# Optimization experiments

Hardware: AMD Instinct MI355X
Metric: run time of the kernel (lower is better)

## Reference

```python
import jax, jax.numpy as jnp
import numpy as np

B_, N, C, NH, NW = 2048, 64, 512, 16, 64  # N == window_size

def setup_inputs() -> dict:
    key = jax.random.key(0)
    k0, k1, k2, k3 = jax.random.split(key, 4)
    std = 0.02
    return {
        "inputs": jax.random.normal(k0, (B_, N, C), jnp.float32),
        "mask": jnp.zeros((NW, N, N), jnp.float32),  # (0 / -inf) additive window mask
        "qkv_w": jax.random.normal(k1, (3 * C, C), jnp.float32) * std,
        "qkv_b": jnp.zeros((3 * C,), jnp.float32),
        "proj_w": jax.random.normal(k2, (C, C), jnp.float32) * std,
        "proj_b": jnp.zeros((C,), jnp.float32),
        "bias_table": jax.random.normal(k3, (2 * N - 1, NH), jnp.float32) * std,
    }

def reference(inputs, mask, qkv_w, qkv_b, proj_w, proj_b, bias_table):
    b, n, c = inputs.shape
    nh = bias_table.shape[1]
    hd = c // nh
    scale = hd ** -0.5
    # qkv projection -> (3, B_, nh, N, hd)
    qkv = (inputs @ qkv_w.T + qkv_b).reshape(b, n, 3, nh, hd).transpose(2, 0, 3, 1, 4)
    q, k, v = qkv[0] * scale, qkv[1], qkv[2]
    attn = jnp.einsum('bhqd,bhkd->bhqk', q, k)  # (B_, nh, N, N)
    # 1D relative position bias, gathered from table
    rel_idx = jnp.arange(n)[:, None] - jnp.arange(n)[None, :] + (n - 1)  # (N, N)
    rel_bias = bias_table[rel_idx]                 # (N, N, nh)
    attn = attn + rel_bias.transpose(2, 0, 1)[None]  # add (nh, N, N)
    # additive window mask
    nw = mask.shape[0]
    attn = attn.reshape(b // nw, nw, nh, n, n) + mask[None, :, None]
    attn = jax.nn.softmax(attn.reshape(b, nh, n, n), axis=-1)
    out = jnp.einsum('bhqk,bhkd->bqhd', attn, v).reshape(b, n, c)
    return out @ proj_w.T + proj_b
```

## Files before the change

### kernel.cpp

```cpp
#include <hip/hip_runtime.h>

typedef __bf16 bf16x8 __attribute__((ext_vector_type(8)));
typedef float f32x4 __attribute__((ext_vector_type(4)));

__device__ __forceinline__ unsigned short f2bf(float x) {
  union { float f; unsigned int u; } c; c.f = x;
  unsigned int r = c.u + 0x7FFFu + ((c.u >> 16) & 1u);
  return (unsigned short)(r >> 16);
}

__global__ __launch_bounds__(256) void f32_to_bf16_vec4(
    const float* __restrict__ in, unsigned short* __restrict__ out, int n4) {
  int i = blockIdx.x * blockDim.x + threadIdx.x;
  int stride = gridDim.x * blockDim.x;
  const float4* in4 = (const float4*)in;
  ushort4* out4 = (ushort4*)out;
  for (; i < n4; i += stride) {
    float4 f = in4[i];
    ushort4 u;
    u.x = f2bf(f.x); u.y = f2bf(f.y); u.z = f2bf(f.z); u.w = f2bf(f.w);
    out4[i] = u;
  }
}

__global__ __launch_bounds__(256) void build_bias_mask_frag(
    const float* __restrict__ bias_table,
    const float* __restrict__ mask,
    float* __restrict__ Mc) {
  const int idx = blockIdx.x * 256 + threadIdx.x;
  const int j = idx & 15, lane = (idx >> 4) & 63, mt = (idx >> 10) & 3;
  const int h = (idx >> 12) & 15, w = idx >> 16;
  const int r = j >> 2, nt = j & 3, lg = lane >> 4, lr = lane & 15;
  const int q = mt * 16 + lg * 4 + r, k = nt * 16 + lr;
  Mc[idx] = bias_table[(q - k + 63) * 16 + h] + mask[(w * 64 + q) * 64 + k];
}

#define GLOAD_LDS16(gp, lp)                                                          \
  __builtin_amdgcn_global_load_lds(                                                  \
      (const __attribute__((address_space(1))) unsigned int*)(uintptr_t)(gp),        \
      (__attribute__((address_space(3))) unsigned int*)(uintptr_t)(lp), 16, 0, 0)

template <int NBN, int EPI>
__global__ __launch_bounds__(512, 2) void gemm256(
    const unsigned short* __restrict__ A,
    const unsigned short* __restrict__ B,
    const float* __restrict__ bias,
    void* __restrict__ C0, void* __restrict__ C1, void* __restrict__ C2,
    int ldc) {
  constexpr int K = 512;
  constexpr int NT = K / 64;
  __shared__ __attribute__((aligned(128))) char lds[131072];

  const int t = threadIdx.x;
  const int lane = t & 63;
  const int wid = t >> 6;
  const int wr = wid >> 2, wc = wid & 3;
  const int lr = lane & 15, lg = lane >> 4;

  const int nwg = gridDim.x;
  const int cpx = nwg >> 3;
  const int wgid = (blockIdx.x & 7) * cpx + (blockIdx.x >> 3);
  const int bm = wgid / NBN, bn = wgid % NBN;
  const int m0 = bm * 256, n0 = bn * 256;

  const char* Ab = (const char*)(A + (size_t)m0 * K);
  const char* Bb = (const char*)(B + (size_t)n0 * K);

  const int r3 = t >> 3, ps = t & 7;

  unsigned aoff[2][2], adst[2][2], boff[2][2], bdst[2][2];
#pragma unroll
  for (int j = 0; j < 2; ++j)
#pragma unroll
    for (int i = 0; i < 2; ++i) {
      const int rowA = i * 128 + j * 64 + r3;
      aoff[j][i] = (unsigned)((rowA * K + ((ps ^ (rowA & 7)) << 3)) * 2);
      adst[j][i] = (unsigned)(rowA * 128 + ps * 16);
      const int rowB = i * 128 + ((r3 >> 5) << 6) + j * 32 + (r3 & 31);
      boff[j][i] = (unsigned)((rowB * K + ((ps ^ (rowB & 7)) << 3)) * 2);
      bdst[j][i] = (unsigned)(65536 + rowB * 128 + ps * 16);
    }

#define STAGE_A(j, tt, buf)                                                   \
  do {                                                                        \
    GLOAD_LDS16(Ab + aoff[j][0] + (tt)*128, lds + (buf)*32768 + adst[j][0]);  \
    GLOAD_LDS16(Ab + aoff[j][1] + (tt)*128, lds + (buf)*32768 + adst[j][1]);  \
  } while (0)
#define STAGE_B(j, tt, buf)                                                   \
  do {                                                                        \
    GLOAD_LDS16(Bb + boff[j][0] + (tt)*128, lds + (buf)*32768 + bdst[j][0]);  \
    GLOAD_LDS16(Bb + boff[j][1] + (tt)*128, lds + (buf)*32768 + bdst[j][1]);  \
  } while (0)

  unsigned abase[2], bbase[2];
#pragma unroll
  for (int kk = 0; kk < 2; ++kk) {
    abase[kk] = (unsigned)((wr * 128 + lr) * 128 + (((kk * 4 + lg) ^ (lr & 7)) << 4));
    bbase[kk] = (unsigned)(65536 + (wc * 64 + lr) * 128 + (((kk * 4 + lg) ^ (lr & 7)) << 4));
  }

  f32x4 acc[8][4];
#pragma unroll
  for (int i = 0; i < 8; ++i)
#pragma unroll
    for (int j = 0; j < 4; ++j) acc[i][j] = f32x4{0.f, 0.f, 0.f, 0.f};

#define BAR_IN()                                         \
  __builtin_amdgcn_s_barrier();                          \
  asm volatile("s_waitcnt lgkmcnt(0)" ::: "memory");     \
  __builtin_amdgcn_sched_barrier(0);                     \
  __builtin_amdgcn_s_setprio(1)
#define MFMA16(QM, NTLO)                                                            \
  _Pragma("unroll") for (int mt = 0; mt < 4; ++mt)                                  \
    _Pragma("unroll") for (int nt = 0; nt < 2; ++nt)                                \
      _Pragma("unroll") for (int kk = 0; kk < 2; ++kk)                              \
        acc[(QM)*4 + mt][(NTLO) + nt] = __builtin_amdgcn_mfma_f32_16x16x32_bf16(    \
            af[mt][kk], bfr[(NTLO) + nt][kk], acc[(QM)*4 + mt][(NTLO) + nt], 0, 0, 0)

  STAGE_A(0, 0, 0); STAGE_B(0, 0, 0); STAGE_B(1, 0, 0); STAGE_A(1, 0, 0);
  STAGE_A(0, 1, 1); STAGE_B(0, 1, 1); STAGE_B(1, 1, 1); STAGE_A(1, 1, 1);
  asm volatile("s_waitcnt vmcnt(8)" ::: "memory");
  __builtin_amdgcn_s_barrier();

#pragma unroll
  for (int tt = 0; tt < NT; ++tt) {
    const int buf = tt & 1;
    bf16x8 af[4][2], bfr[4][2];
#pragma unroll
    for (int nt = 0; nt < 2; ++nt)
#pragma unroll
      for (int kk = 0; kk < 2; ++kk)
        bfr[nt][kk] = *(const bf16x8*)(lds + buf * 32768 + bbase[kk] + nt * 2048);
#pragma unroll
    for (int mt = 0; mt < 4; ++mt)
#pragma unroll
      for (int kk = 0; kk < 2; ++kk)
        af[mt][kk] = *(const bf16x8*)(lds + buf * 32768 + abase[kk] + mt * 2048);
    BAR_IN();
    MFMA16(0, 0);
    __builtin_amdgcn_s_setprio(0);
    __builtin_amdgcn_s_barrier();
#pragma unroll
    for (int nt = 2; nt < 4; ++nt)
#pragma unroll
      for (int kk = 0; kk < 2; ++kk)
        bfr[nt][kk] = *(const bf16x8*)(lds + buf * 32768 + bbase[kk] + nt * 2048);
    if (tt + 2 < NT) { STAGE_A(0, tt + 2, buf); STAGE_B(0, tt + 2, buf); }
    BAR_IN();
    MFMA16(0, 2);
    __builtin_amdgcn_s_setprio(0);
    __builtin_amdgcn_s_barrier();
#pragma unroll
    for (int mt = 0; mt < 4; ++mt)
#pragma unroll
      for (int kk = 0; kk < 2; ++kk)
        af[mt][kk] = *(const bf16x8*)(lds + buf * 32768 + abase[kk] + 8192 + mt * 2048);
    if (tt + 2 < NT) STAGE_B(1, tt + 2, buf);
    BAR_IN();
    MFMA16(1, 0);
    __builtin_amdgcn_s_setprio(0);
    __builtin_amdgcn_s_barrier();
    if (tt + 2 < NT) STAGE_A(1, tt + 2, buf);
    BAR_IN();
    MFMA16(1, 2);
    __builtin_amdgcn_s_setprio(0);
    if (tt + 2 < NT)      asm volatile("s_waitcnt vmcnt(8)" ::: "memory");
    else if (tt == NT - 2) asm volatile("s_waitcnt vmcnt(0)" ::: "memory");
    __builtin_amdgcn_s_barrier();
  }
#undef MFMA16
#undef BAR_IN
#undef STAGE_A
#undef STAGE_B

#pragma unroll
  for (int qm = 0; qm < 2; ++qm)
#pragma unroll
    for (int mt = 0; mt < 4; ++mt)
#pragma unroll
      for (int nt = 0; nt < 4; ++nt) {
        const int n = n0 + wc * 64 + nt * 16 + lr;
        const float bv = bias[n];
        const f32x4 a4 = acc[qm * 4 + mt][nt];
        if constexpr (EPI == 2) {
          const int part = n >> 9;
          unsigned short* dst = part == 0 ? (unsigned short*)C0
                                 : (part == 1 ? (unsigned short*)C1 : (unsigned short*)C2);
          const float sc = (part == 0) ? 0.17677669529663687f : 1.0f;
          const int hh = (n >> 5) & 15, dd = n & 31;
#pragma unroll
          for (int r = 0; r < 4; ++r) {
            const int m = m0 + wr * 128 + qm * 64 + mt * 16 + lg * 4 + r;
            dst[((size_t)((m >> 6) * 16 + hh) * 64 + (m & 63)) * 32 + dd] =
                f2bf((a4[r] + bv) * sc);
          }
        } else {
#pragma unroll
          for (int r = 0; r < 4; ++r) {
            const int m = m0 + wr * 128 + qm * 64 + mt * 16 + lg * 4 + r;
            ((float*)C0)[(size_t)m * ldc + n] = a4[r] + bv;
          }
        }
      }
}

__global__ __launch_bounds__(128) void attn_kernel(
    const unsigned short* __restrict__ Qh,
    const unsigned short* __restrict__ Kh,
    const unsigned short* __restrict__ Vh,
    const float* __restrict__ Mc,
    unsigned short* __restrict__ attn_out
) {
  const int wv = threadIdx.x >> 6;
  const int bh = blockIdx.x * 2 + wv;
  const int b = bh >> 4, h = bh & 15;
  const int lane = threadIdx.x & 63;
  const int lr = lane & 15, lg = lane >> 4;

  __shared__ unsigned short VtS[2][32 * 72];
  __shared__ unsigned short PlS[2][16 * 72];
  unsigned short* Vt = VtS[wv];
  unsigned short* Pl = PlS[wv];

  const unsigned short* qb = Qh + (size_t)bh * 2048;
  const unsigned short* kb = Kh + (size_t)bh * 2048;
  const unsigned short* vg = Vh + (size_t)bh * 2048;

  bf16x8 vr[4];
#pragma unroll
  for (int i = 0; i < 4; ++i) vr[i] = ((const bf16x8*)(vg + lane * 32))[i];
  bf16x8 kf[4], qf[4];
#pragma unroll
  for (int nt = 0; nt < 4; ++nt)
    kf[nt] = *(const bf16x8*)(kb + (nt * 16 + lr) * 32 + lg * 8);
#pragma unroll
  for (int mt = 0; mt < 4; ++mt)
    qf[mt] = *(const bf16x8*)(qb + (mt * 16 + lr) * 32 + lg * 8);

  {
    __bf16* vt = (__bf16*)Vt;
#pragma unroll
    for (int d = 0; d < 8; ++d) {
      vt[(d)*72 + lane] = vr[0][d];
      vt[(d + 8) * 72 + lane] = vr[1][d];
      vt[(d + 16) * 72 + lane] = vr[2][d];
      vt[(d + 24) * 72 + lane] = vr[3][d];
    }
  }
  bf16x8 vfrag[2][2];
#pragma unroll
  for (int dt = 0; dt < 2; ++dt)
#pragma unroll
    for (int ki = 0; ki < 2; ++ki)
      vfrag[dt][ki] = *(const bf16x8*)(Vt + (dt * 16 + lr) * 72 + ki * 32 + lg * 8);

  const float* Mb = Mc + ((size_t)((b & 63) * 16 + h) * 4) * 1024 + lane * 16;

  f32x4 o[4][2];
#pragma unroll
  for (int i = 0; i < 4; ++i)
#pragma unroll
    for (int j = 0; j < 2; ++j) o[i][j] = f32x4{0.f, 0.f, 0.f, 0.f};
  float rinv[4][4];

#pragma unroll
  for (int mt = 0; mt < 4; ++mt) {
    f32x4 mv4[4];
#pragma unroll
    for (int j = 0; j < 4; ++j)
      mv4[j] = ((const f32x4*)(Mb + (size_t)mt * 1024))[j];

    f32x4 s[4];
#pragma unroll
    for (int nt = 0; nt < 4; ++nt) s[nt] = f32x4{0.f, 0.f, 0.f, 0.f};
#pragma unroll
    for (int nt = 0; nt < 4; ++nt)
      s[nt] = __builtin_amdgcn_mfma_f32_16x16x32_bf16(qf[mt], kf[nt], s[nt], 0, 0, 0);

#pragma unroll
    for (int r = 0; r < 4; ++r) {
      float v[4];
      float sum = 0.f;
#pragma unroll
      for (int nt = 0; nt < 4; ++nt) {
        v[nt] = __expf(s[nt][r] + mv4[r][nt]);
        sum += v[nt];
      }
      sum += __shfl_xor(sum, 1, 64);
      sum += __shfl_xor(sum, 2, 64);
      sum += __shfl_xor(sum, 4, 64);
      sum += __shfl_xor(sum, 8, 64);
      rinv[mt][r] = __builtin_amdgcn_rcpf(sum);
#pragma unroll
      for (int nt = 0; nt < 4; ++nt)
        Pl[(lg * 4 + r) * 72 + nt * 16 + lr] = f2bf(v[nt]);
    }

    bf16x8 pa[2];
#pragma unroll
    for (int ki = 0; ki < 2; ++ki)
      pa[ki] = *(const bf16x8*)(Pl + lr * 72 + ki * 32 + lg * 8);
#pragma unroll
    for (int dt = 0; dt < 2; ++dt)
#pragma unroll
      for (int ki = 0; ki < 2; ++ki)
        o[mt][dt] = __builtin_amdgcn_mfma_f32_16x16x32_bf16(pa[ki], vfrag[dt][ki], o[mt][dt], 0, 0, 0);
  }

#pragma unroll
  for (int mt = 0; mt < 4; ++mt) {
#pragma unroll
    for (int r = 0; r < 4; ++r) {
      const int m = mt * 16 + lg * 4 + r;
      const float ri = rinv[mt][r];
#pragma unroll
      for (int dt = 0; dt < 2; ++dt) {
        const int d = dt * 16 + lr;
        attn_out[(size_t)(b * 64 + m) * 512 + h * 32 + d] = f2bf(o[mt][dt][r] * ri);
      }
    }
  }
}

extern "C" void kernel_launch(void* const* d_in, const int* in_sizes, int n_in,
                              void* d_out, int out_size, void* d_ws, size_t ws_size,
                              hipStream_t stream) {
  const float* X = (const float*)d_in[0];
  const float* mask = (const float*)d_in[1];
  const float* qkv_w = (const float*)d_in[2];
  const float* qkv_b = (const float*)d_in[3];
  const float* proj_w = (const float*)d_in[4];
  const float* proj_b = (const float*)d_in[5];
  const float* bias_table = (const float*)d_in[6];
  float* out = (float*)d_out;
  char* ws = (char*)d_ws;

  unsigned short* Xb      = (unsigned short*)(ws);
  unsigned short* Qh      = (unsigned short*)(ws + 134217728ull);
  unsigned short* Kh      = (unsigned short*)(ws + 268435456ull);
  unsigned short* Vh      = (unsigned short*)(ws + 402653184ull);
  unsigned short* attnout = (unsigned short*)(ws + 536870912ull);
  unsigned short* qkv_wb  = (unsigned short*)(ws + 671088640ull);
  unsigned short* proj_wb = (unsigned short*)(ws + 672661504ull);
  float*          Mf      = (float*)(ws + 673185792ull);

  f32_to_bf16_vec4<<<2048, 256, 0, stream>>>(X, Xb, 67108864 / 4);
  f32_to_bf16_vec4<<<768, 256, 0, stream>>>(qkv_w, qkv_wb, 786432 / 4);
  f32_to_bf16_vec4<<<256, 256, 0, stream>>>(proj_w, proj_wb, 262144 / 4);
  build_bias_mask_frag<<<16384, 256, 0, stream>>>(bias_table, mask, Mf);

  gemm256<6, 2><<<3072, 512, 0, stream>>>(Xb, qkv_wb, qkv_b, (void*)Qh, (void*)Kh, (void*)Vh, 1536);

  attn_kernel<<<16384, 128, 0, stream>>>(Qh, Kh, Vh, Mf, attnout);

  gemm256<2, 0><<<1024, 512, 0, stream>>>(attnout, proj_wb, proj_b, (void*)out, nullptr, nullptr, 512);
}
```

Baseline: 635.6 us.

## Rebalance GEMM prefetch schedule and transpose attention scores for cheaper softmax

The GEMM main loop now prefetches the second half of the next K tile into the other buffer during the current iteration and the first half two iterations ahead, with adjusted vmcnt waits. This spreads global-to-LDS loads more evenly across the MFMA phases. The attention kernel computes S transposed (K×Q), so each lane holds four key values for one query row. That cuts the row-sum reduction to two cross-lane shuffles, lets P be normalised before packing with v_cvt_pk_bf16_f32 and written as 8-byte stores, and removes the final rescale. The bias/mask fragment layout is permuted to match, and the new wait counts carry a risk of ordering errors.

```diff
diff --git a/kernel.cpp b/kernel.cpp
--- a/kernel.cpp
+++ b/kernel.cpp
@@ -7,6 +7,12 @@
   union { float f; unsigned int u; } c; c.f = x;
   unsigned int r = c.u + 0x7FFFu + ((c.u >> 16) & 1u);
   return (unsigned short)(r >> 16);
+}
+
+__device__ __forceinline__ unsigned int cvt_pk_bf16(float a, float b) {
+  unsigned int r;
+  asm("v_cvt_pk_bf16_f32 %0, %1, %2" : "=v"(r) : "v"(a), "v"(b));
+  return r;
 }
 
 __global__ __launch_bounds__(256) void f32_to_bf16_vec4(
@@ -30,8 +36,8 @@
   const int idx = blockIdx.x * 256 + threadIdx.x;
   const int j = idx & 15, lane = (idx >> 4) & 63, mt = (idx >> 10) & 3;
   const int h = (idx >> 12) & 15, w = idx >> 16;
-  const int r = j >> 2, nt = j & 3, lg = lane >> 4, lr = lane & 15;
-  const int q = mt * 16 + lg * 4 + r, k = nt * 16 + lr;
+  const int nt = j >> 2, r = j & 3, lg = lane >> 4, lr = lane & 15;
+  const int q = mt * 16 + lr, k = nt * 16 + lg * 4 + r;
   Mc[idx] = bias_table[(q - k + 63) * 16 + h] + mask[(w * 64 + q) * 64 + k];
 }
 
@@ -118,13 +124,14 @@
             af[mt][kk], bfr[(NTLO) + nt][kk], acc[(QM)*4 + mt][(NTLO) + nt], 0, 0, 0)
 
   STAGE_A(0, 0, 0); STAGE_B(0, 0, 0); STAGE_B(1, 0, 0); STAGE_A(1, 0, 0);
-  STAGE_A(0, 1, 1); STAGE_B(0, 1, 1); STAGE_B(1, 1, 1); STAGE_A(1, 1, 1);
+  STAGE_A(0, 1, 1); STAGE_B(0, 1, 1);
   asm volatile("s_waitcnt vmcnt(8)" ::: "memory");
   __builtin_amdgcn_s_barrier();
 
 #pragma unroll
   for (int tt = 0; tt < NT; ++tt) {
     const int buf = tt & 1;
+    const int nb = buf ^ 1;
     bf16x8 af[4][2], bfr[4][2];
 #pragma unroll
     for (int nt = 0; nt < 2; ++nt)
@@ -136,36 +143,42 @@
 #pragma unroll
       for (int kk = 0; kk < 2; ++kk)
         af[mt][kk] = *(const bf16x8*)(lds + buf * 32768 + abase[kk] + mt * 2048);
+    if (tt + 1 < NT) STAGE_B(1, tt + 1, nb);
     BAR_IN();
     MFMA16(0, 0);
     __builtin_amdgcn_s_setprio(0);
+    if (tt == NT - 1) asm volatile("s_waitcnt vmcnt(2)" ::: "memory");
+    else              asm volatile("s_waitcnt vmcnt(8)" ::: "memory");
     __builtin_amdgcn_s_barrier();
 #pragma unroll
     for (int nt = 2; nt < 4; ++nt)
 #pragma unroll
       for (int kk = 0; kk < 2; ++kk)
         bfr[nt][kk] = *(const bf16x8*)(lds + buf * 32768 + bbase[kk] + nt * 2048);
-    if (tt + 2 < NT) { STAGE_A(0, tt + 2, buf); STAGE_B(0, tt + 2, buf); }
+    if (tt + 1 < NT) STAGE_A(1, tt + 1, nb);
     BAR_IN();
     MFMA16(0, 2);
     __builtin_amdgcn_s_setprio(0);
+    if (tt == NT - 1) asm volatile("s_waitcnt vmcnt(0)" ::: "memory");
+    else              asm volatile("s_waitcnt vmcnt(8)" ::: "memory");
     __builtin_amdgcn_s_barrier();
 #pragma unroll
     for (int mt = 0; mt < 4; ++mt)
 #pragma unroll
       for (int kk = 0; kk < 2; ++kk)
         af[mt][kk] = *(const bf16x8*)(lds + buf * 32768 + abase[kk] + 8192 + mt * 2048);
-    if (tt + 2 < NT) STAGE_B(1, tt + 2, buf);
+    if (tt + 2 < NT) STAGE_A(0, tt + 2, buf);
     BAR_IN();
     MFMA16(1, 0);
     __builtin_amdgcn_s_setprio(0);
+    if (tt < NT - 1) asm volatile("s_waitcnt vmcnt(8)" ::: "memory");
     __builtin_amdgcn_s_barrier();
-    if (tt + 2 < NT) STAGE_A(1, tt + 2, buf);
+    if (tt + 2 < NT) STAGE_B(0, tt + 2, buf);
     BAR_IN();
     MFMA16(1, 2);
     __builtin_amdgcn_s_setprio(0);
-    if (tt + 2 < NT)      asm volatile("s_waitcnt vmcnt(8)" ::: "memory");
-    else if (tt == NT - 2) asm volatile("s_waitcnt vmcnt(0)" ::: "memory");
+    if (tt < NT - 2)       asm volatile("s_waitcnt vmcnt(8)" ::: "memory");
+    else if (tt == NT - 2) asm volatile("s_waitcnt vmcnt(4)" ::: "memory");
     __builtin_amdgcn_s_barrier();
   }
 #undef MFMA16
@@ -261,39 +274,42 @@
   for (int i = 0; i < 4; ++i)
 #pragma unroll
     for (int j = 0; j < 2; ++j) o[i][j] = f32x4{0.f, 0.f, 0.f, 0.f};
-  float rinv[4][4];
 
 #pragma unroll
   for (int mt = 0; mt < 4; ++mt) {
-    f32x4 mv4[4];
-#pragma unroll
-    for (int j = 0; j < 4; ++j)
-      mv4[j] = ((const f32x4*)(Mb + (size_t)mt * 1024))[j];
-
-    f32x4 s[4];
-#pragma unroll
-    for (int nt = 0; nt < 4; ++nt) s[nt] = f32x4{0.f, 0.f, 0.f, 0.f};
+    f32x4 mv[4];
 #pragma unroll
     for (int nt = 0; nt < 4; ++nt)
-      s[nt] = __builtin_amdgcn_mfma_f32_16x16x32_bf16(qf[mt], kf[nt], s[nt], 0, 0, 0);
-
-#pragma unroll
-    for (int r = 0; r < 4; ++r) {
-      float v[4];
-      float sum = 0.f;
-#pragma unroll
-      for (int nt = 0; nt < 4; ++nt) {
-        v[nt] = __expf(s[nt][r] + mv4[r][nt]);
-        sum += v[nt];
-      }
-      sum += __shfl_xor(sum, 1, 64);
-      sum += __shfl_xor(sum, 2, 64);
-      sum += __shfl_xor(sum, 4, 64);
-      sum += __shfl_xor(sum, 8, 64);
-      rinv[mt][r] = __builtin_amdgcn_rcpf(sum);
-#pragma unroll
-      for (int nt = 0; nt < 4; ++nt)
-        Pl[(lg * 4 + r) * 72 + nt * 16 + lr] = f2bf(v[nt]);
+      mv[nt] = ((const f32x4*)(Mb + (size_t)mt * 1024))[nt];
+
+    f32x4 s2[4];
+#pragma unroll
+    for (int nt = 0; nt < 4; ++nt) s2[nt] = f32x4{0.f, 0.f, 0.f, 0.f};
+#pragma unroll
+    for (int nt = 0; nt < 4; ++nt)
+      s2[nt] = __builtin_amdgcn_mfma_f32_16x16x32_bf16(kf[nt], qf[mt], s2[nt], 0, 0, 0);
+
+    float e[4][4];
+    float ps[4];
+#pragma unroll
+    for (int nt = 0; nt < 4; ++nt) {
+      e[nt][0] = __expf(s2[nt][0] + mv[nt][0]);
+      e[nt][1] = __expf(s2[nt][1] + mv[nt][1]);
+      e[nt][2] = __expf(s2[nt][2] + mv[nt][2]);
+      e[nt][3] = __expf(s2[nt][3] + mv[nt][3]);
+      ps[nt] = (e[nt][0] + e[nt][1]) + (e[nt][2] + e[nt][3]);
+    }
+    float sum = (ps[0] + ps[1]) + (ps[2] + ps[3]);
+    sum += __shfl_xor(sum, 16, 64);
+    sum += __shfl_xor(sum, 32, 64);
+    const float ri = __builtin_amdgcn_rcpf(sum);
+
+#pragma unroll
+    for (int nt = 0; nt < 4; ++nt) {
+      uint2 w2;
+      w2.x = cvt_pk_bf16(e[nt][0] * ri, e[nt][1] * ri);
+      w2.y = cvt_pk_bf16(e[nt][2] * ri, e[nt][3] * ri);
+      *(uint2*)((char*)Pl + lr * 144 + nt * 32 + lg * 8) = w2;
     }
 
     bf16x8 pa[2];
@@ -312,11 +328,10 @@
 #pragma unroll
     for (int r = 0; r < 4; ++r) {
       const int m = mt * 16 + lg * 4 + r;
-      const float ri = rinv[mt][r];
 #pragma unroll
       for (int dt = 0; dt < 2; ++dt) {
         const int d = dt * 16 + lr;
-        attn_out[(size_t)(b * 64 + m) * 512 + h * 32 + d] = f2bf(o[mt][dt][r] * ri);
+        attn_out[(size_t)(b * 64 + m) * 512 + h * 32 + d] = f2bf(o[mt][dt][r]);
       }
     }
   }
```

Measured after the change: 615.7 us. -3.1%, faster.
